# Optimization experiments

Hardware: AMD Instinct MI355X
Metric: run time of the kernel (lower is better)

## Reference

```python
import jax, jax.numpy as jnp
import numpy as np

COMMITMENT_COST = 0.25
NUM_EMBEDDINGS = 4096
EMBEDDING_DIM = 256


def setup_inputs() -> dict:
    key = jax.random.key(0)
    k1, k2 = jax.random.split(key)
    inputs = jax.random.normal(k1, (32, EMBEDDING_DIM, 2048), dtype=jnp.float32)
    # nn.Embedding weight initialized uniform(-1/K, 1/K)
    codebook = jax.random.uniform(
        k2, (NUM_EMBEDDINGS, EMBEDDING_DIM), dtype=jnp.float32,
        minval=-1.0 / NUM_EMBEDDINGS, maxval=1.0 / NUM_EMBEDDINGS)
    return {"inputs": inputs, "codebook": codebook}


def reference(inputs, codebook):
    B, D, S = inputs.shape
    sg = jax.lax.stop_gradient
    # [B, D, S] -> [B*S, D]
    flat = jnp.transpose(inputs, (0, 2, 1)).reshape(-1, D)
    distances = (jnp.sum(flat ** 2, axis=1, keepdims=True)
                 + jnp.sum(codebook ** 2, axis=1)
                 - 2.0 * flat @ codebook.T)
    encoding_indices = jnp.argmin(distances, axis=1)  # [N]
    # direct gather (same math as one-hot @ codebook)
    quantized = codebook[encoding_indices].reshape(B, S, D)
    quantized = jnp.transpose(quantized, (0, 2, 1))  # [B, D, S]
    e_latent_loss = jnp.mean((sg(quantized) - inputs) ** 2)
    q_latent_loss = jnp.mean((quantized - sg(inputs)) ** 2)
    loss = COMMITMENT_COST * e_latent_loss + q_latent_loss
    # straight-through estimator
    quantized_st = inputs + sg(quantized - inputs)
    return quantized_st, loss
```

## Files before the change

kernel.cpp:

```cpp
#include <hip/hip_runtime.h>

#define K_CODES 4096
#define DIM 256
#define SEQ 2048
#define NTOK 65536

typedef __bf16 bf16x8 __attribute__((ext_vector_type(8)));
typedef float floatx4 __attribute__((ext_vector_type(4)));
typedef unsigned short u16x8 __attribute__((ext_vector_type(8)));

__device__ __forceinline__ unsigned short f2bf(float f) {
    union { float f; unsigned int u; } v; v.f = f;
    unsigned int u = v.u;
    unsigned int r = u + 0x7fffu + ((u >> 16) & 1u);
    return (unsigned short)(r >> 16);
}

__global__ __launch_bounds__(256) void k_prep(const float* __restrict__ cb,
        unsigned short* __restrict__ cb_swz, float* __restrict__ norms,
        float* __restrict__ loss_slot) {
    const int c = blockIdx.x;
    const int t = threadIdx.x;
    const int row_loc = t >> 3;
    const int ks = t & 7;
    const int row = c * 32 + row_loc;
    const float* src = cb + (size_t)row * DIM + ks * 32;
    float vals[32];
    float s = 0.0f;
    #pragma unroll
    for (int i = 0; i < 8; ++i) {
        floatx4 v = *(const floatx4*)(src + i * 4);
        #pragma unroll
        for (int j = 0; j < 4; ++j) { vals[i * 4 + j] = v[j]; s += v[j] * v[j]; }
    }
    const int ns = row_loc >> 4, col = row_loc & 15;
    #pragma unroll
    for (int quad = 0; quad < 4; ++quad) {
        u16x8 p;
        #pragma unroll
        for (int j = 0; j < 8; ++j) p[j] = f2bf(vals[quad * 8 + j]);
        *(u16x8*)(cb_swz + ((size_t)((c * 16 + ns * 8 + ks) * 64 + quad * 16 + col)) * 8) = p;
    }
    s += __shfl_xor(s, 1); s += __shfl_xor(s, 2); s += __shfl_xor(s, 4);
    if (ks == 0) norms[row] = s + 1.0f;
    if (c == 0 && t == 0) *loss_slot = 0.0f;
}

__global__ __launch_bounds__(64, 2) void k_argmin(const float* __restrict__ x,
        const unsigned short* __restrict__ cb_swz, const float* __restrict__ norms,
        unsigned int* __restrict__ halfmin) {
    __shared__ __align__(16) unsigned short xs[8448];
    const int lane = threadIdx.x;
    const int col = lane & 15, quad = lane >> 4;
    const int bx = blockIdx.x;
    const int h = bx & 1;
    const int tok0 = (bx >> 1) * 64;
    const int b = tok0 >> 11, s0 = tok0 & 2047;
    const float* xin = x + (size_t)b * DIM * SEQ;

    bf16x8 af[4][8];
    const int dl = lane >> 3, so = (lane & 7) * 4;
    for (int sub = 0; sub < 2; ++sub) {
        const int sbase = s0 + sub * 32;
        for (int i = 0; i < 32; ++i) {
            int d = i * 8 + dl;
            floatx4 v = *(const floatx4*)(xin + (size_t)d * SEQ + sbase + so);
            #pragma unroll
            for (int j = 0; j < 4; ++j) xs[(so + j) * 264 + d] = f2bf(-2.0f * v[j]);
        }
        __builtin_amdgcn_s_waitcnt(0);
        #pragma unroll
        for (int mm = 0; mm < 2; ++mm)
            #pragma unroll
            for (int ks = 0; ks < 8; ++ks)
                af[sub * 2 + mm][ks] =
                    *(const bf16x8*)&xs[(mm * 16 + col) * 264 + quad * 8 + ks * 32];
        __builtin_amdgcn_s_waitcnt(0);
    }

    unsigned int minkey[4][4];
    #pragma unroll
    for (int m = 0; m < 4; ++m)
        #pragma unroll
        for (int r = 0; r < 4; ++r) minkey[m][r] = 0xFFFFFFFFu;

    for (int c = 0; c < 64; ++c) {
        const int gc = h * 64 + c;
        #pragma unroll
        for (int ns = 0; ns < 2; ++ns) {
            const float nv = norms[gc * 32 + ns * 16 + col];
            bf16x8 bfrag[8];
            #pragma unroll
            for (int ks = 0; ks < 8; ++ks)
                bfrag[ks] = *(const bf16x8*)(cb_swz +
                    ((size_t)((gc * 16 + ns * 8 + ks) * 64) + lane) * 8);
            floatx4 acc[4];
            #pragma unroll
            for (int m = 0; m < 4; ++m) acc[m] = (floatx4){nv, nv, nv, nv};
            #pragma unroll
            for (int ks = 0; ks < 8; ++ks)
                #pragma unroll
                for (int m = 0; m < 4; ++m)
                    acc[m] = __builtin_amdgcn_mfma_f32_16x16x32_bf16(
                                 af[m][ks], bfrag[ks], acc[m], 0, 0, 0);
            const unsigned int code = gc * 32 + ns * 16 + col;
            #pragma unroll
            for (int m = 0; m < 4; ++m)
                #pragma unroll
                for (int r = 0; r < 4; ++r) {
                    unsigned int key = (__float_as_uint(acc[m][r]) & 0xFFFFF000u) | code;
                    minkey[m][r] = key < minkey[m][r] ? key : minkey[m][r];
                }
        }
    }

    #pragma unroll
    for (int m = 0; m < 4; ++m)
        #pragma unroll
        for (int r = 0; r < 4; ++r) {
            unsigned int k = minkey[m][r];
            #pragma unroll
            for (int off = 8; off >= 1; off >>= 1) {
                unsigned int o = __shfl_xor(k, off);
                k = o < k ? o : k;
            }
            if (col == 0)
                halfmin[h * NTOK + tok0 + m * 16 + quad * 4 + r] = k;
        }
}

__global__ __launch_bounds__(512) void k_gather(const float* __restrict__ x,
        const float* __restrict__ cb, const unsigned int* __restrict__ halfmin,
        float* __restrict__ out, float* __restrict__ loss_slot) {
    __shared__ __align__(16) float qs[256 * 64];
    __shared__ int sidx[64];
    __shared__ float wpart[8];
    const int t = threadIdx.x;
    const int tb = blockIdx.x * 64;
    const int b = tb >> 11, s0 = tb & 2047;
    if (t < 64) {
        unsigned int p0 = halfmin[tb + t], p1 = halfmin[NTOK + tb + t];
        sidx[t] = (int)((p0 < p1 ? p0 : p1) & 0xFFFu);
    }
    __syncthreads();
    {
        const int tl = t >> 3, seg = t & 7;
        const float* src = cb + (size_t)sidx[tl] * DIM + seg * 32;
        const int pos = (tl + seg * 8) & 63;
        #pragma unroll
        for (int i = 0; i < 8; ++i) {
            floatx4 v = *(const floatx4*)(src + i * 4);
            #pragma unroll
            for (int j = 0; j < 4; ++j) qs[(seg * 32 + i * 4 + j) * 64 + pos] = v[j];
        }
    }
    __syncthreads();
    float acc = 0.0f;
    {
        const int d0 = t >> 4, j0 = (t & 15) * 4;
        #pragma unroll
        for (int dd = 0; dd < 8; ++dd) {
            int d = dd * 32 + d0;
            size_t g = (size_t)b * DIM * SEQ + (size_t)d * SEQ + s0 + j0;
            floatx4 xv = *(const floatx4*)(x + g);
            floatx4 qv = *(const floatx4*)&qs[d * 64 + ((j0 + (d >> 5) * 8) & 63)];
            *(floatx4*)(out + g) = qv;
            floatx4 df = qv - xv;
            acc += df[0]*df[0] + df[1]*df[1] + df[2]*df[2] + df[3]*df[3];
        }
    }
    for (int off = 32; off; off >>= 1) acc += __shfl_xor(acc, off);
    if ((t & 63) == 0) wpart[t >> 6] = acc;
    __syncthreads();
    if (t == 0) {
        float tot = 0.0f;
        #pragma unroll
        for (int i = 0; i < 8; ++i) tot += wpart[i];
        atomicAdd(loss_slot, tot * (1.25f / 16777216.0f));
    }
}

extern "C" void kernel_launch(void* const* d_in, const int* in_sizes, int n_in,
                              void* d_out, int out_size, void* d_ws, size_t ws_size,
                              hipStream_t stream) {
    const float* inputs   = (const float*)d_in[0];
    const float* codebook = (const float*)d_in[1];
    float* out = (float*)d_out;
    unsigned short* cb_swz = (unsigned short*)d_ws;
    float* norms = (float*)((char*)d_ws + (size_t)K_CODES * DIM * 2);
    unsigned int* halfmin = (unsigned int*)((char*)d_ws + (size_t)K_CODES * DIM * 2
                                            + K_CODES * 4);
    float* loss_slot = out + (out_size - 1);

    hipLaunchKernelGGL(k_prep,   dim3(K_CODES / 32), dim3(256), 0, stream,
                       codebook, cb_swz, norms, loss_slot);
    hipLaunchKernelGGL(k_argmin, dim3(NTOK / 64 * 2), dim3(64), 0, stream,
                       inputs, cb_swz, norms, halfmin);
    hipLaunchKernelGGL(k_gather, dim3(NTOK / 64), dim3(512), 0, stream,
                       inputs, codebook, halfmin, out, loss_slot);
}
```

Before: 281.6 us.

## Fuse argmin and gather kernels; compute loss from min distance; double-buffer codebook loads

Merges the argmin and gather kernels into one 128-thread block per 64 tokens, where each wave scans half the codebook and the two half-minima are combined in shared memory. The loss is now taken from the minimum distance plus the token's squared norm instead of re-reading x and differencing, which removes a full input read. Codebook fragments are software double-buffered across iterations. In exchange the loss uses bf16-rounded, truncated distances, which costs accuracy. The output is written from a small per-pass transpose buffer, and the larger per-block shared memory may lower occupancy.

```diff
diff --git a/kernel.cpp b/kernel.cpp
--- a/kernel.cpp
+++ b/kernel.cpp
@@ -46,37 +46,54 @@
     if (c == 0 && t == 0) *loss_slot = 0.0f;
 }
 
-__global__ __launch_bounds__(64, 2) void k_argmin(const float* __restrict__ x,
+__global__ __launch_bounds__(128, 2) void k_main(const float* __restrict__ x,
         const unsigned short* __restrict__ cb_swz, const float* __restrict__ norms,
-        unsigned int* __restrict__ halfmin) {
-    __shared__ __align__(16) unsigned short xs[8448];
-    const int lane = threadIdx.x;
+        const float* __restrict__ cb, float* __restrict__ out,
+        float* __restrict__ loss_slot) {
+    __shared__ __align__(16) unsigned short xs[2][8448];
+    __shared__ __align__(16) float qs[16 * 260];
+    __shared__ unsigned int mkey[2][64];
+    __shared__ float sumx2s[64];
+    __shared__ int sidx[64];
+
+    const int t = threadIdx.x;
+    const int lane = t & 63, w = t >> 6;
     const int col = lane & 15, quad = lane >> 4;
-    const int bx = blockIdx.x;
-    const int h = bx & 1;
-    const int tok0 = (bx >> 1) * 64;
+    const int h = w;
+    const int tok0 = blockIdx.x * 64;
     const int b = tok0 >> 11, s0 = tok0 & 2047;
     const float* xin = x + (size_t)b * DIM * SEQ;
 
-    bf16x8 af[4][8];
     const int dl = lane >> 3, so = (lane & 7) * 4;
-    for (int sub = 0; sub < 2; ++sub) {
-        const int sbase = s0 + sub * 32;
+    {
+        const int sbase = s0 + w * 32;
+        floatx4 a2 = {0.0f, 0.0f, 0.0f, 0.0f};
         for (int i = 0; i < 32; ++i) {
             int d = i * 8 + dl;
             floatx4 v = *(const floatx4*)(xin + (size_t)d * SEQ + sbase + so);
-            #pragma unroll
-            for (int j = 0; j < 4; ++j) xs[(so + j) * 264 + d] = f2bf(-2.0f * v[j]);
-        }
-        __builtin_amdgcn_s_waitcnt(0);
-        #pragma unroll
-        for (int mm = 0; mm < 2; ++mm)
+            a2 += v * v;
+            #pragma unroll
+            for (int j = 0; j < 4; ++j) xs[w][(so + j) * 264 + d] = f2bf(-2.0f * v[j]);
+        }
+        #pragma unroll
+        for (int off = 8; off <= 32; off <<= 1)
+            #pragma unroll
+            for (int j = 0; j < 4; ++j) a2[j] += __shfl_xor(a2[j], off);
+        if (dl == 0)
+            #pragma unroll
+            for (int j = 0; j < 4; ++j) sumx2s[w * 32 + (lane & 7) * 4 + j] = a2[j];
+    }
+    __syncthreads();
+
+    bf16x8 af[4][8];
+    #pragma unroll
+    for (int sub = 0; sub < 2; ++sub)
+        #pragma unroll
+        for (int m2 = 0; m2 < 2; ++m2)
             #pragma unroll
             for (int ks = 0; ks < 8; ++ks)
-                af[sub * 2 + mm][ks] =
-                    *(const bf16x8*)&xs[(mm * 16 + col) * 264 + quad * 8 + ks * 32];
-        __builtin_amdgcn_s_waitcnt(0);
-    }
+                af[sub * 2 + m2][ks] =
+                    *(const bf16x8*)&xs[sub][(m2 * 16 + col) * 264 + quad * 8 + ks * 32];
 
     unsigned int minkey[4][4];
     #pragma unroll
@@ -84,34 +101,45 @@
         #pragma unroll
         for (int r = 0; r < 4; ++r) minkey[m][r] = 0xFFFFFFFFu;
 
+    const unsigned short* cbb = cb_swz + (size_t)h * 1024 * 512 + lane * 8;
+
+    auto ldb = [&](bf16x8* dst, int it) {
+        const unsigned short* p = cbb + (size_t)it * 8 * 512;
+        #pragma unroll
+        for (int ks = 0; ks < 8; ++ks) dst[ks] = *(const bf16x8*)(p + ks * 512);
+    };
+    auto compute = [&](const bf16x8* buf, float nv, int it) {
+        floatx4 acc[4];
+        #pragma unroll
+        for (int m = 0; m < 4; ++m) acc[m] = (floatx4){nv, nv, nv, nv};
+        #pragma unroll
+        for (int ks = 0; ks < 8; ++ks)
+            #pragma unroll
+            for (int m = 0; m < 4; ++m)
+                acc[m] = __builtin_amdgcn_mfma_f32_16x16x32_bf16(
+                             af[m][ks], buf[ks], acc[m], 0, 0, 0);
+        const unsigned int code = (unsigned int)(h * 2048 + it * 16 + col);
+        #pragma unroll
+        for (int m = 0; m < 4; ++m)
+            #pragma unroll
+            for (int r = 0; r < 4; ++r) {
+                unsigned int key = (__float_as_uint(acc[m][r]) & 0xFFFFF000u) | code;
+                minkey[m][r] = key < minkey[m][r] ? key : minkey[m][r];
+            }
+    };
+
+    bf16x8 bA[8], bB[8];
+    float nvA = norms[h * 2048 + col], nvB;
+    ldb(bA, 0);
     for (int c = 0; c < 64; ++c) {
-        const int gc = h * 64 + c;
-        #pragma unroll
-        for (int ns = 0; ns < 2; ++ns) {
-            const float nv = norms[gc * 32 + ns * 16 + col];
-            bf16x8 bfrag[8];
-            #pragma unroll
-            for (int ks = 0; ks < 8; ++ks)
-                bfrag[ks] = *(const bf16x8*)(cb_swz +
-                    ((size_t)((gc * 16 + ns * 8 + ks) * 64) + lane) * 8);
-            floatx4 acc[4];
-            #pragma unroll
-            for (int m = 0; m < 4; ++m) acc[m] = (floatx4){nv, nv, nv, nv};
-            #pragma unroll
-            for (int ks = 0; ks < 8; ++ks)
-                #pragma unroll
-                for (int m = 0; m < 4; ++m)
-                    acc[m] = __builtin_amdgcn_mfma_f32_16x16x32_bf16(
-                                 af[m][ks], bfrag[ks], acc[m], 0, 0, 0);
-            const unsigned int code = gc * 32 + ns * 16 + col;
-            #pragma unroll
-            for (int m = 0; m < 4; ++m)
-                #pragma unroll
-                for (int r = 0; r < 4; ++r) {
-                    unsigned int key = (__float_as_uint(acc[m][r]) & 0xFFFFF000u) | code;
-                    minkey[m][r] = key < minkey[m][r] ? key : minkey[m][r];
-                }
-        }
+        const int it = c * 2;
+        nvB = norms[h * 2048 + (it + 1) * 16 + col];
+        ldb(bB, it + 1);
+        compute(bA, nvA, it);
+        const int itn = (it + 2) & 127;
+        nvA = norms[h * 2048 + itn * 16 + col];
+        ldb(bA, itn);
+        compute(bB, nvB, it + 1);
     }
 
     #pragma unroll
@@ -124,59 +152,42 @@
                 unsigned int o = __shfl_xor(k, off);
                 k = o < k ? o : k;
             }
-            if (col == 0)
-                halfmin[h * NTOK + tok0 + m * 16 + quad * 4 + r] = k;
-        }
-}
-
-__global__ __launch_bounds__(512) void k_gather(const float* __restrict__ x,
-        const float* __restrict__ cb, const unsigned int* __restrict__ halfmin,
-        float* __restrict__ out, float* __restrict__ loss_slot) {
-    __shared__ __align__(16) float qs[256 * 64];
-    __shared__ int sidx[64];
-    __shared__ float wpart[8];
-    const int t = threadIdx.x;
-    const int tb = blockIdx.x * 64;
-    const int b = tb >> 11, s0 = tb & 2047;
+            if (col == 0) mkey[w][m * 16 + quad * 4 + r] = k;
+        }
+    __syncthreads();
+
     if (t < 64) {
-        unsigned int p0 = halfmin[tb + t], p1 = halfmin[NTOK + tb + t];
-        sidx[t] = (int)((p0 < p1 ? p0 : p1) & 0xFFFu);
-    }
-    __syncthreads();
-    {
-        const int tl = t >> 3, seg = t & 7;
-        const float* src = cb + (size_t)sidx[tl] * DIM + seg * 32;
-        const int pos = (tl + seg * 8) & 63;
-        #pragma unroll
-        for (int i = 0; i < 8; ++i) {
-            floatx4 v = *(const floatx4*)(src + i * 4);
-            #pragma unroll
-            for (int j = 0; j < 4; ++j) qs[(seg * 32 + i * 4 + j) * 64 + pos] = v[j];
-        }
-    }
-    __syncthreads();
-    float acc = 0.0f;
-    {
-        const int d0 = t >> 4, j0 = (t & 15) * 4;
-        #pragma unroll
-        for (int dd = 0; dd < 8; ++dd) {
-            int d = dd * 32 + d0;
-            size_t g = (size_t)b * DIM * SEQ + (size_t)d * SEQ + s0 + j0;
-            floatx4 xv = *(const floatx4*)(x + g);
-            floatx4 qv = *(const floatx4*)&qs[d * 64 + ((j0 + (d >> 5) * 8) & 63)];
-            *(floatx4*)(out + g) = qv;
-            floatx4 df = qv - xv;
-            acc += df[0]*df[0] + df[1]*df[1] + df[2]*df[2] + df[3]*df[3];
-        }
-    }
-    for (int off = 32; off; off >>= 1) acc += __shfl_xor(acc, off);
-    if ((t & 63) == 0) wpart[t >> 6] = acc;
-    __syncthreads();
-    if (t == 0) {
-        float tot = 0.0f;
-        #pragma unroll
-        for (int i = 0; i < 8; ++i) tot += wpart[i];
-        atomicAdd(loss_slot, tot * (1.25f / 16777216.0f));
+        unsigned int k0 = mkey[0][t], k1 = mkey[1][t];
+        unsigned int km = k0 < k1 ? k0 : k1;
+        sidx[t] = (int)(km & 0xFFFu);
+        float dtok = __uint_as_float(km & 0xFFFFF000u) - 1.0f + sumx2s[t];
+        #pragma unroll
+        for (int off = 32; off; off >>= 1) dtok += __shfl_xor(dtok, off);
+        if (t == 0) atomicAdd(loss_slot, dtok * (1.25f / 16777216.0f));
+    }
+
+    for (int pass = 0; pass < 4; ++pass) {
+        __syncthreads();
+        {
+            const int tl = t >> 3, seg = t & 7;
+            const float* src = cb + (size_t)sidx[pass * 16 + tl] * DIM + seg * 32;
+            #pragma unroll
+            for (int i = 0; i < 8; ++i)
+                *(floatx4*)&qs[tl * 260 + seg * 32 + i * 4] = *(const floatx4*)(src + i * 4);
+        }
+        __syncthreads();
+        {
+            const int d0 = t >> 2, a = t & 3;
+            #pragma unroll
+            for (int p = 0; p < 8; ++p) {
+                const int d = p * 32 + d0;
+                floatx4 q;
+                #pragma unroll
+                for (int j = 0; j < 4; ++j) q[j] = qs[(a * 4 + j) * 260 + d];
+                *(floatx4*)(out + (size_t)b * DIM * SEQ + (size_t)d * SEQ
+                            + s0 + pass * 16 + a * 4) = q;
+            }
+        }
     }
 }
 
@@ -188,14 +199,10 @@
     float* out = (float*)d_out;
     unsigned short* cb_swz = (unsigned short*)d_ws;
     float* norms = (float*)((char*)d_ws + (size_t)K_CODES * DIM * 2);
-    unsigned int* halfmin = (unsigned int*)((char*)d_ws + (size_t)K_CODES * DIM * 2
-                                            + K_CODES * 4);
     float* loss_slot = out + (out_size - 1);
 
-    hipLaunchKernelGGL(k_prep,   dim3(K_CODES / 32), dim3(256), 0, stream,
+    hipLaunchKernelGGL(k_prep, dim3(K_CODES / 32), dim3(256), 0, stream,
                        codebook, cb_swz, norms, loss_slot);
-    hipLaunchKernelGGL(k_argmin, dim3(NTOK / 64 * 2), dim3(64), 0, stream,
-                       inputs, cb_swz, norms, halfmin);
-    hipLaunchKernelGGL(k_gather, dim3(NTOK / 64), dim3(512), 0, stream,
-                       inputs, codebook, halfmin, out, loss_slot);
-}
+    hipLaunchKernelGGL(k_main, dim3(NTOK / 64), dim3(128), 0, stream,
+                       inputs, cb_swz, norms, codebook, out, loss_slot);
+}
```

New measurement: 374.1 us. 32.9% more time.

## Stage codebook tiles in LDS via async copies and compute loss from distances

Applied to the files above, without the earlier changes.

The argmin kernel now runs 256-thread blocks of four waves that share each codebook chunk. Chunks are double-buffered in LDS with global_load_lds async copies instead of every wave reading them from global memory. The loss is computed algebraically from the min distance key plus ||x||^2, accumulated while loading x, so the gather kernel no longer re-reads the inputs. The gather writes codebook rows straight to the output without an LDS transpose. The trade-offs are lower loss precision, since the key keeps truncated mantissa bits of bf16-based distances, and more sync points in the main loop.

```diff
diff --git a/kernel.cpp b/kernel.cpp
--- a/kernel.cpp
+++ b/kernel.cpp
@@ -14,6 +14,15 @@
     unsigned int u = v.u;
     unsigned int r = u + 0x7fffu + ((u >> 16) & 1u);
     return (unsigned short)(r >> 16);
+}
+
+__device__ __forceinline__ void async_cp16(const void* g, const void* lds_base) {
+    typedef __attribute__((address_space(1))) const unsigned int guint;
+    typedef __attribute__((address_space(3))) unsigned int luint;
+    __builtin_amdgcn_global_load_lds(
+        (guint*)(unsigned long long)g,
+        (luint*)(unsigned int)(unsigned long long)lds_base,
+        16, 0, 0);
 }
 
 __global__ __launch_bounds__(256) void k_prep(const float* __restrict__ cb,
@@ -42,58 +51,89 @@
         *(u16x8*)(cb_swz + ((size_t)((c * 16 + ns * 8 + ks) * 64 + quad * 16 + col)) * 8) = p;
     }
     s += __shfl_xor(s, 1); s += __shfl_xor(s, 2); s += __shfl_xor(s, 4);
-    if (ks == 0) norms[row] = s + 1.0f;
+    if (ks == 0) norms[row] = s + 0.25f;
     if (c == 0 && t == 0) *loss_slot = 0.0f;
 }
 
-__global__ __launch_bounds__(64, 2) void k_argmin(const float* __restrict__ x,
+__global__ __launch_bounds__(256, 2) void k_argmin(const float* __restrict__ x,
         const unsigned short* __restrict__ cb_swz, const float* __restrict__ norms,
-        unsigned int* __restrict__ halfmin) {
-    __shared__ __align__(16) unsigned short xs[8448];
-    const int lane = threadIdx.x;
+        unsigned int* __restrict__ halfmin, float* __restrict__ loss_slot) {
+    __shared__ __align__(16) unsigned short xs[64 * 264];
+    __shared__ __align__(16) unsigned short ring[2][8192];
+    __shared__ float wpart[4];
+    const int t = threadIdx.x;
+    const int lane = t & 63, w = t >> 6;
     const int col = lane & 15, quad = lane >> 4;
     const int bx = blockIdx.x;
     const int h = bx & 1;
-    const int tok0 = (bx >> 1) * 64;
-    const int b = tok0 >> 11, s0 = tok0 & 2047;
+    const int tb = (bx >> 1) * 256;
+    const int b = tb >> 11, s0 = tb & 2047;
     const float* xin = x + (size_t)b * DIM * SEQ;
 
+    {
+        const char* src = (const char*)cb_swz + (size_t)h * 64 * 16384;
+        #pragma unroll
+        for (int i = 0; i < 4; ++i)
+            async_cp16(src + i * 4096 + w * 1024 + lane * 16,
+                       (char*)ring[0] + i * 4096 + w * 1024);
+    }
+
     bf16x8 af[4][8];
-    const int dl = lane >> 3, so = (lane & 7) * 4;
-    for (int sub = 0; sub < 2; ++sub) {
-        const int sbase = s0 + sub * 32;
-        for (int i = 0; i < 32; ++i) {
-            int d = i * 8 + dl;
-            floatx4 v = *(const floatx4*)(xin + (size_t)d * SEQ + sbase + so);
-            #pragma unroll
-            for (int j = 0; j < 4; ++j) xs[(so + j) * 264 + d] = f2bf(-2.0f * v[j]);
-        }
-        __builtin_amdgcn_s_waitcnt(0);
-        #pragma unroll
-        for (int mm = 0; mm < 2; ++mm)
+    float a2 = 0.0f;
+    const int dg = t >> 4, sq = (t & 15) * 4;
+    for (int ph = 0; ph < 4; ++ph) {
+        const int sbase = s0 + ph * 64 + sq;
+        for (int i = 0; i < 16; ++i) {
+            int d = i * 16 + dg;
+            floatx4 v = *(const floatx4*)(xin + (size_t)d * SEQ + sbase);
+            a2 += v[0]*v[0] + v[1]*v[1] + v[2]*v[2] + v[3]*v[3];
+            #pragma unroll
+            for (int j = 0; j < 4; ++j) xs[(sq + j) * 264 + d] = f2bf(-2.0f * v[j]);
+        }
+        __syncthreads();
+        if (w == ph) {
+            #pragma unroll
+            for (int m = 0; m < 4; ++m)
+                #pragma unroll
+                for (int ks = 0; ks < 8; ++ks)
+                    af[m][ks] = *(const bf16x8*)&xs[(m * 16 + col) * 264
+                                                    + quad * 8 + ks * 32];
+        }
+        __syncthreads();
+    }
+    #pragma unroll
+    for (int off = 1; off < 64; off <<= 1) a2 += __shfl_xor(a2, off);
+    if (lane == 0) wpart[w] = a2;
+    __syncthreads();
+    if (t == 0 && h == 0)
+        atomicAdd(loss_slot,
+                  (wpart[0] + wpart[1] + wpart[2] + wpart[3]) * (1.25f / 16777216.0f));
+
+    unsigned int minkey[4][4];
+    #pragma unroll
+    for (int m = 0; m < 4; ++m)
+        #pragma unroll
+        for (int r = 0; r < 4; ++r) minkey[m][r] = 0xFFFFFFFFu;
+
+    #pragma unroll 1
+    for (int c = 0; c < 64; ++c) {
+        __syncthreads();
+        if (c < 63) {
+            const char* src = (const char*)cb_swz + (size_t)(h * 64 + c + 1) * 16384;
+            char* dst = (char*)ring[(c + 1) & 1];
+            #pragma unroll
+            for (int i = 0; i < 4; ++i)
+                async_cp16(src + i * 4096 + w * 1024 + lane * 16,
+                           dst + i * 4096 + w * 1024);
+        }
+        const unsigned short* buf = ring[c & 1];
+        #pragma unroll
+        for (int ns = 0; ns < 2; ++ns) {
+            const float nv = norms[(h * 64 + c) * 32 + ns * 16 + col];
+            bf16x8 bfrag[8];
             #pragma unroll
             for (int ks = 0; ks < 8; ++ks)
-                af[sub * 2 + mm][ks] =
-                    *(const bf16x8*)&xs[(mm * 16 + col) * 264 + quad * 8 + ks * 32];
-        __builtin_amdgcn_s_waitcnt(0);
-    }
-
-    unsigned int minkey[4][4];
-    #pragma unroll
-    for (int m = 0; m < 4; ++m)
-        #pragma unroll
-        for (int r = 0; r < 4; ++r) minkey[m][r] = 0xFFFFFFFFu;
-
-    for (int c = 0; c < 64; ++c) {
-        const int gc = h * 64 + c;
-        #pragma unroll
-        for (int ns = 0; ns < 2; ++ns) {
-            const float nv = norms[gc * 32 + ns * 16 + col];
-            bf16x8 bfrag[8];
-            #pragma unroll
-            for (int ks = 0; ks < 8; ++ks)
-                bfrag[ks] = *(const bf16x8*)(cb_swz +
-                    ((size_t)((gc * 16 + ns * 8 + ks) * 64) + lane) * 8);
+                bfrag[ks] = *(const bf16x8*)&buf[((ns * 8 + ks) * 64 + lane) * 8];
             floatx4 acc[4];
             #pragma unroll
             for (int m = 0; m < 4; ++m) acc[m] = (floatx4){nv, nv, nv, nv};
@@ -103,7 +143,7 @@
                 for (int m = 0; m < 4; ++m)
                     acc[m] = __builtin_amdgcn_mfma_f32_16x16x32_bf16(
                                  af[m][ks], bfrag[ks], acc[m], 0, 0, 0);
-            const unsigned int code = gc * 32 + ns * 16 + col;
+            const unsigned int code = (unsigned int)((h * 64 + c) * 32 + ns * 16 + col);
             #pragma unroll
             for (int m = 0; m < 4; ++m)
                 #pragma unroll
@@ -125,58 +165,38 @@
                 k = o < k ? o : k;
             }
             if (col == 0)
-                halfmin[h * NTOK + tok0 + m * 16 + quad * 4 + r] = k;
-        }
-}
-
-__global__ __launch_bounds__(512) void k_gather(const float* __restrict__ x,
-        const float* __restrict__ cb, const unsigned int* __restrict__ halfmin,
-        float* __restrict__ out, float* __restrict__ loss_slot) {
-    __shared__ __align__(16) float qs[256 * 64];
+                halfmin[h * NTOK + tb + w * 64 + m * 16 + quad * 4 + r] = k;
+        }
+}
+
+__global__ __launch_bounds__(256) void k_gather(const float* __restrict__ cb,
+        const unsigned int* __restrict__ halfmin, float* __restrict__ out,
+        float* __restrict__ loss_slot) {
     __shared__ int sidx[64];
-    __shared__ float wpart[8];
     const int t = threadIdx.x;
     const int tb = blockIdx.x * 64;
     const int b = tb >> 11, s0 = tb & 2047;
     if (t < 64) {
-        unsigned int p0 = halfmin[tb + t], p1 = halfmin[NTOK + tb + t];
-        sidx[t] = (int)((p0 < p1 ? p0 : p1) & 0xFFFu);
+        unsigned int k0 = halfmin[tb + t], k1 = halfmin[NTOK + tb + t];
+        unsigned int km = k0 < k1 ? k0 : k1;
+        sidx[t] = (int)(km & 0xFFFu);
+        float dv = __uint_as_float(km & 0xFFFFF000u) - 0.25f;
+        #pragma unroll
+        for (int off = 32; off; off >>= 1) dv += __shfl_xor(dv, off);
+        if (t == 0) atomicAdd(loss_slot, dv * (1.25f / 16777216.0f));
     }
     __syncthreads();
-    {
-        const int tl = t >> 3, seg = t & 7;
-        const float* src = cb + (size_t)sidx[tl] * DIM + seg * 32;
-        const int pos = (tl + seg * 8) & 63;
-        #pragma unroll
-        for (int i = 0; i < 8; ++i) {
-            floatx4 v = *(const floatx4*)(src + i * 4);
-            #pragma unroll
-            for (int j = 0; j < 4; ++j) qs[(seg * 32 + i * 4 + j) * 64 + pos] = v[j];
-        }
-    }
-    __syncthreads();
-    float acc = 0.0f;
-    {
-        const int d0 = t >> 4, j0 = (t & 15) * 4;
-        #pragma unroll
-        for (int dd = 0; dd < 8; ++dd) {
-            int d = dd * 32 + d0;
-            size_t g = (size_t)b * DIM * SEQ + (size_t)d * SEQ + s0 + j0;
-            floatx4 xv = *(const floatx4*)(x + g);
-            floatx4 qv = *(const floatx4*)&qs[d * 64 + ((j0 + (d >> 5) * 8) & 63)];
-            *(floatx4*)(out + g) = qv;
-            floatx4 df = qv - xv;
-            acc += df[0]*df[0] + df[1]*df[1] + df[2]*df[2] + df[3]*df[3];
-        }
-    }
-    for (int off = 32; off; off >>= 1) acc += __shfl_xor(acc, off);
-    if ((t & 63) == 0) wpart[t >> 6] = acc;
-    __syncthreads();
-    if (t == 0) {
-        float tot = 0.0f;
-        #pragma unroll
-        for (int i = 0; i < 8; ++i) tot += wpart[i];
-        atomicAdd(loss_slot, tot * (1.25f / 16777216.0f));
+    const int q = t & 15, dg = t >> 4;
+    int rows[4];
+    #pragma unroll
+    for (int k = 0; k < 4; ++k) rows[k] = sidx[q * 4 + k];
+    #pragma unroll
+    for (int i = 0; i < 16; ++i) {
+        const int d = i * 16 + dg;
+        floatx4 v;
+        #pragma unroll
+        for (int k = 0; k < 4; ++k) v[k] = cb[(size_t)rows[k] * DIM + d];
+        *(floatx4*)(out + (size_t)b * DIM * SEQ + (size_t)d * SEQ + s0 + q * 4) = v;
     }
 }
 
@@ -192,10 +212,10 @@
                                             + K_CODES * 4);
     float* loss_slot = out + (out_size - 1);
 
-    hipLaunchKernelGGL(k_prep,   dim3(K_CODES / 32), dim3(256), 0, stream,
+    hipLaunchKernelGGL(k_prep,   dim3(K_CODES / 32),     dim3(256), 0, stream,
                        codebook, cb_swz, norms, loss_slot);
-    hipLaunchKernelGGL(k_argmin, dim3(NTOK / 64 * 2), dim3(64), 0, stream,
-                       inputs, cb_swz, norms, halfmin);
-    hipLaunchKernelGGL(k_gather, dim3(NTOK / 64), dim3(512), 0, stream,
-                       inputs, codebook, halfmin, out, loss_slot);
-}
+    hipLaunchKernelGGL(k_argmin, dim3(NTOK / 256 * 2),   dim3(256), 0, stream,
+                       inputs, cb_swz, norms, halfmin, loss_slot);
+    hipLaunchKernelGGL(k_gather, dim3(NTOK / 64),        dim3(256), 0, stream,
+                       codebook, halfmin, out, loss_slot);
+}
```

Result: faster. 262.0 us (-7.0%).
